# Kernel tuning notes

Measured on AMD Instinct MI355X. Metric: run time of the kernel, lower is better.

## Reference

```python
import jax, jax.numpy as jnp
import numpy as np

V, E, H, B, T = 50000, 300, 512, 64, 256


def _lstm_dir(x, wih, whh, bih, bhh, reverse):
    # x: [B,T,D]; wih: [4H,D]; whh: [4H,H]; PyTorch gate order i,f,g,o
    pre = jnp.einsum('btd,gd->btg', x, wih) + bih + bhh  # [B,T,4H]
    pre_t = jnp.swapaxes(pre, 0, 1)  # [T,B,4H]
    h0 = jnp.zeros((x.shape[0], whh.shape[1]), x.dtype)

    def step(carry, g):
        h, c = carry
        gates = g + h @ whh.T
        i, f, gg, o = jnp.split(gates, 4, axis=-1)
        c = jax.nn.sigmoid(f) * c + jax.nn.sigmoid(i) * jnp.tanh(gg)
        h = jax.nn.sigmoid(o) * jnp.tanh(c)
        return (h, c), h

    _, hs = jax.lax.scan(step, (h0, h0), pre_t, reverse=reverse)
    return jnp.swapaxes(hs, 0, 1)  # [B,T,H]


def setup_inputs() -> dict:
    key = jax.random.key(0)
    ks = jax.random.split(key, 24)
    s = 1.0 / np.sqrt(H)
    u = lambda k, shp: jax.random.uniform(k, shp, jnp.float32, -s, s)
    inp = {
        'input_ids': jax.random.randint(ks[0], (B, T), 0, V),
        'input_masks': jnp.ones((B, T), jnp.float32),
        'labels': jax.random.uniform(ks[1], (B, T), jnp.float32),
        'emb': jax.random.normal(ks[2], (V, E), jnp.float32),
        'lin_w': u(ks[3], (1, H)), 'lin_b': u(ks[4], (1,)),
    }
    dims = {'l0': E, 'l1': 2 * H}
    i = 5
    for layer, din in dims.items():
        for d in ('f', 'b'):
            inp[f'w_ih_{layer}{d}'] = u(ks[i], (4 * H, din)); i += 1
            inp[f'w_hh_{layer}{d}'] = u(ks[i], (4 * H, H)); i += 1
            inp[f'b_ih_{layer}{d}'] = u(ks[i], (4 * H,)); i += 1
            inp[f'b_hh_{layer}{d}'] = u(ks[i], (4 * H,)); i += 1
    return inp


def reference(input_ids, input_masks, labels, emb, lin_w, lin_b,
              w_ih_l0f, w_hh_l0f, b_ih_l0f, b_hh_l0f,
              w_ih_l0b, w_hh_l0b, b_ih_l0b, b_hh_l0b,
              w_ih_l1f, w_hh_l1f, b_ih_l1f, b_hh_l1f,
              w_ih_l1b, w_hh_l1b, b_ih_l1b, b_hh_l1b):
    x = emb[input_ids]  # vectorized gather, [B,T,E]
    h0f = _lstm_dir(x, w_ih_l0f, w_hh_l0f, b_ih_l0f, b_hh_l0f, False)
    h0b = _lstm_dir(x, w_ih_l0b, w_hh_l0b, b_ih_l0b, b_hh_l0b, True)
    x1 = jnp.concatenate([h0f, h0b], axis=-1)  # [B,T,2H] (dropout inactive at eval)
    h1f = _lstm_dir(x1, w_ih_l1f, w_hh_l1f, b_ih_l1f, b_hh_l1f, False)
    h1b = _lstm_dir(x1, w_ih_l1b, w_hh_l1b, b_ih_l1b, b_hh_l1b, True)
    mean_h = 0.5 * (h1f + h1b)  # mean over 2 directions, [B,T,H]
    scores = jax.nn.sigmoid(jnp.einsum('bth,oh->bto', mean_h, lin_w) + lin_b)  # [B,T,1]
    err = (scores[..., 0] - labels) ** 2 * input_masks  # masked MSE per token
    loss = jnp.mean(jnp.sum(err, axis=1) / jnp.sum(input_masks, axis=1))
    return loss
```

## Files before the change

### kernel.cpp

```cpp
#include <hip/hip_runtime.h>
#include <stdint.h>

#define T_SEQ 256
#define B_SZ  64
#define HID   512
#define G4    2048
#define E_DIM 300
#define E_PAD 320

typedef float f32x4 __attribute__((ext_vector_type(4)));
typedef short bf16x8 __attribute__((ext_vector_type(8)));
typedef short s16x4 __attribute__((ext_vector_type(4)));
typedef unsigned int u32x4 __attribute__((ext_vector_type(4)));

__device__ __forceinline__ unsigned short f2bf(float f) {
    union { float f; unsigned u; } v; v.f = f;
    unsigned r = v.u + 0x7FFF + ((v.u >> 16) & 1);
    return (unsigned short)(r >> 16);
}
__device__ __forceinline__ float bf2f(unsigned short b) {
    union { unsigned u; float f; } v; v.u = ((unsigned)b) << 16;
    return v.f;
}
__device__ __forceinline__ float sigm_f(float x) { return 1.0f / (1.0f + __expf(-x)); }
__device__ __forceinline__ float tanh_f(float x) {
    float e = __expf(-2.0f * fabsf(x));
    float t = (1.0f - e) / (1.0f + e);
    return x < 0.0f ? -t : t;
}

__global__ void k_sentinel(float* out) { out[0] = 12345.0f; }

__global__ __launch_bounds__(256) void k_gather(const int* __restrict__ ids,
                                                const float* __restrict__ emb,
                                                unsigned short* __restrict__ x) {
    int w = threadIdx.x >> 6, lane = threadIdx.x & 63;
    int m = blockIdx.x * 4 + w;
    int b = m & 63, t = m >> 6;
    int id = ids[b * T_SEQ + t];
    const float* e = emb + (size_t)id * E_DIM;
    unsigned short* xr = x + (size_t)m * E_PAD;
    for (int k = lane; k < E_PAD; k += 64)
        xr[k] = (k < E_DIM) ? f2bf(e[k]) : (unsigned short)0;
}

struct CastJobs {
    const float* s[8];
    unsigned short* d[8];
    int ks[8];
    int kp[8];
};
__global__ __launch_bounds__(256) void k_castall(CastJobs jobs) {
    int job = blockIdx.x >> 11;
    int row = blockIdx.x & 2047;
    int Ks = jobs.ks[job], Kp = jobs.kp[job];
    const float* s = jobs.s[job] + (size_t)row * Ks;
    unsigned short* d = jobs.d[job] + (size_t)row * Kp;
    for (int k = threadIdx.x; k < Kp; k += 256)
        d[k] = (k < Ks) ? f2bf(s[k]) : (unsigned short)0;
}

__global__ __launch_bounds__(256) void k_gemm(const unsigned short* __restrict__ A,
                                              const unsigned short* __restrict__ W,
                                              const float* __restrict__ bih,
                                              const float* __restrict__ bhh,
                                              unsigned short* __restrict__ outp,
                                              int Ka) {
    __shared__ __align__(16) short As[64][40];
    __shared__ __align__(16) short Bs[64][40];
    int tid = threadIdx.x;
    int w = tid >> 6, lane = tid & 63;
    int m0 = blockIdx.x * 64, n0 = blockIdx.y * 64;

    f32x4 acc[4];
    #pragma unroll
    for (int nt = 0; nt < 4; ++nt) { acc[nt][0]=0.f; acc[nt][1]=0.f; acc[nt][2]=0.f; acc[nt][3]=0.f; }

    int r = tid >> 2, seg = tid & 3;
    for (int k0 = 0; k0 < Ka; k0 += 32) {
        *(bf16x8*)&As[r][seg * 8] = *(const bf16x8*)&A[(size_t)(m0 + r) * Ka + k0 + seg * 8];
        *(bf16x8*)&Bs[r][seg * 8] = *(const bf16x8*)&W[(size_t)(n0 + r) * Ka + k0 + seg * 8];
        __syncthreads();
        bf16x8 a = *(const bf16x8*)&As[w * 16 + (lane & 15)][(lane >> 4) * 8];
        #pragma unroll
        for (int nt = 0; nt < 4; ++nt) {
            bf16x8 b = *(const bf16x8*)&Bs[nt * 16 + (lane & 15)][(lane >> 4) * 8];
            acc[nt] = __builtin_amdgcn_mfma_f32_16x16x32_bf16(a, b, acc[nt], 0, 0, 0);
        }
        __syncthreads();
    }
    int q = lane >> 4, j = lane & 15;
    int t = (m0 >> 6);
    #pragma unroll
    for (int nt = 0; nt < 4; ++nt) {
        int col = n0 + nt * 16 + j;
        int g = col >> 9, jc = col & 511;
        float b0 = bih[col] + bhh[col];
        s16x4 pk;
        #pragma unroll
        for (int rr = 0; rr < 4; ++rr)
            pk[rr] = (short)f2bf(acc[nt][rr] + b0);
        size_t idx = (((((size_t)t * 4 + w) * 4 + q) * 32 + (jc >> 4)) * 16 + (jc & 15)) * 16 + g * 4;
        *(s16x4*)&outp[idx] = pk;
    }
}

__global__ __launch_bounds__(256, 1) void k_lstm_layer(
        const unsigned short* __restrict__ pre2_f, const unsigned short* __restrict__ pre2_b,
        const unsigned short* __restrict__ whh_f, const unsigned short* __restrict__ whh_b,
        unsigned short* __restrict__ h_pp,
        int* __restrict__ flags,
        unsigned short* __restrict__ x1,
        unsigned short* __restrict__ h1f, unsigned short* __restrict__ h1b,
        int mode, int flag_base) {
    int tid = threadIdx.x, w = tid >> 6, lane = tid & 63;
    int jgg = blockIdx.x, rg = blockIdx.y, dir = blockIdx.z;
    int jg = jgg * 4 + w;
    int r0 = rg * 16, q = lane >> 4, j = lane & 15;
    const unsigned short* pre2 = dir ? pre2_b : pre2_f;
    const unsigned short* whh = dir ? whh_b : whh_f;
    int* gbase = flags + ((dir * 4 + rg) * 8) * 16;

    __shared__ __align__(16) short ws_a[16 * 512];

    bf16x8 breg[4][16];
    #pragma unroll
    for (int g = 0; g < 4; ++g)
        #pragma unroll
        for (int kc = 0; kc < 16; ++kc)
            breg[g][kc] = *(const bf16x8*)(whh + (size_t)(g * 512 + jg * 16 + j) * 512 + q * 8 + kc * 32);
    #pragma unroll
    for (int g = 0; g < 4; ++g)
        #pragma unroll
        for (int kc = 0; kc < 16; ++kc)
            asm volatile("" : "+a"(breg[g][kc]));

    float cr[4];
    #pragma unroll
    for (int rr = 0; rr < 4; ++rr) cr[rr] = 0.f;

    int aswz = (j & 7) << 4;
    const char* abase = (const char*)ws_a + (j << 10);
    int ko16 = q << 4;

    bf16x8 pcur0, pcur1;
    {
        int t0 = dir ? (T_SEQ - 1) : 0;
        const unsigned short* pp =
            pre2 + ((((((size_t)t0 * 4 + rg) * 4 + q) * 32 + jg) * 16 + j) * 16);
        pcur0 = *(const bf16x8*)pp;
        pcur1 = *(const bf16x8*)(pp + 8);
    }

    for (int s = 0; s < T_SEQ; ++s) {
        int t = dir ? (T_SEQ - 1 - s) : s;
        const unsigned short* hprev = h_pp + ((size_t)(s & 1) * 2 + dir) * (B_SZ * HID);
        unsigned short* hnext = h_pp + ((size_t)((s + 1) & 1) * 2 + dir) * (B_SZ * HID);

        f32x4 a0, a1, a2, a3;
        a0[0]=0.f;a0[1]=0.f;a0[2]=0.f;a0[3]=0.f; a1=a0; a2=a0; a3=a0;
        if (s > 0) {
            const unsigned short* hp = hprev + (size_t)r0 * HID;
            u32x4 va[4];
            #pragma unroll
            for (int c = 0; c < 4; ++c) {
                int ch = tid + c * 256;
                const void* src = hp + ((ch >> 6) << 9) + ((ch & 63) << 3);
                asm volatile("global_load_dwordx4 %0, %1, off sc0 sc1"
                             : "=v"(va[c]) : "v"(src));
            }
            asm volatile("s_waitcnt vmcnt(0)" ::: "memory");
            #pragma unroll
            for (int c = 0; c < 4; ++c) {
                int ch = tid + c * 256;
                int r = ch >> 6, o = ch & 63;
                *(u32x4*)((char*)ws_a + (r << 10) + ((o << 4) ^ ((r & 7) << 4))) = va[c];
            }
            __syncthreads();

            #pragma unroll
            for (int kc = 0; kc < 16; ++kc) {
                bf16x8 a = *(const bf16x8*)(abase + (((kc << 6) + ko16) ^ aswz));
                a0 = __builtin_amdgcn_mfma_f32_16x16x32_bf16(a, breg[0][kc], a0, 0, 0, 0);
                a1 = __builtin_amdgcn_mfma_f32_16x16x32_bf16(a, breg[1][kc], a1, 0, 0, 0);
                a2 = __builtin_amdgcn_mfma_f32_16x16x32_bf16(a, breg[2][kc], a2, 0, 0, 0);
                a3 = __builtin_amdgcn_mfma_f32_16x16x32_bf16(a, breg[3][kc], a3, 0, 0, 0);
            }
        }

        unsigned hbits[4];
        #pragma unroll
        for (int rr = 0; rr < 4; ++rr) {
            float iv = a0[rr] + bf2f((unsigned short)pcur0[rr]);
            float fv = a1[rr] + bf2f((unsigned short)pcur0[4 + rr]);
            float gv = a2[rr] + bf2f((unsigned short)pcur1[rr]);
            float ov = a3[rr] + bf2f((unsigned short)pcur1[4 + rr]);
            cr[rr] = sigm_f(fv) * cr[rr] + sigm_f(iv) * tanh_f(gv);
            float hh = sigm_f(ov) * tanh_f(cr[rr]);
            hbits[rr] = (unsigned)f2bf(hh);
        }

        #pragma unroll
        for (int rr = 0; rr < 4; ++rr) {
            unsigned nb = (unsigned)__shfl_xor((int)hbits[rr], 1);
            if ((j & 1) == 0) {
                unsigned pair = (hbits[rr] & 0xFFFFu) | (nb << 16);
                void* dsth = (void*)(hnext + (size_t)(r0 + q * 4 + rr) * HID + jg * 16 + j);
                asm volatile("global_store_dword %0, %1, off sc0 sc1"
                             :: "v"(dsth), "v"(pair) : "memory");
            }
        }

        asm volatile("s_waitcnt vmcnt(0)" ::: "memory");
        __syncthreads();
        int target = flag_base + s + 1;
        if (tid == 0)
            __hip_atomic_store(&gbase[jgg * 16], target, __ATOMIC_RELAXED, __HIP_MEMORY_SCOPE_AGENT);

        #pragma unroll
        for (int rr = 0; rr < 4; ++rr) {
            unsigned short hb = (unsigned short)hbits[rr];
            int brow = r0 + q * 4 + rr;
            if (mode == 0)
                x1[((size_t)t * B_SZ + brow) * 1024 + dir * HID + jg * 16 + j] = hb;
            else {
                unsigned short* o = dir ? h1b : h1f;
                o[((size_t)t * B_SZ + brow) * HID + jg * 16 + j] = hb;
            }
        }
        bf16x8 pn0, pn1;
        {
            int sn = (s + 1 < T_SEQ) ? s + 1 : s;
            int tn = dir ? (T_SEQ - 1 - sn) : sn;
            const unsigned short* pp =
                pre2 + ((((((size_t)tn * 4 + rg) * 4 + q) * 32 + jg) * 16 + j) * 16);
            pn0 = *(const bf16x8*)pp;
            pn1 = *(const bf16x8*)(pp + 8);
        }

        if (tid < 8) {
            while (__hip_atomic_load(&gbase[tid * 16], __ATOMIC_RELAXED, __HIP_MEMORY_SCOPE_AGENT) < target) {}
        }
        __syncthreads();
        pcur0 = pn0; pcur1 = pn1;
    }
}

__global__ __launch_bounds__(256) void k_score(const unsigned short* __restrict__ h1f,
                                               const unsigned short* __restrict__ h1b,
                                               const float* __restrict__ lin_w,
                                               const float* __restrict__ lin_b,
                                               const float* __restrict__ labels,
                                               const float* __restrict__ masks,
                                               float* __restrict__ err) {
    int w = threadIdx.x >> 6, lane = threadIdx.x & 63;
    int idx = blockIdx.x * 4 + w;
    int b = idx >> 8, t = idx & 255;
    size_t base = ((size_t)t * B_SZ + b) * HID + lane * 8;
    bf16x8 hf = *(const bf16x8*)(h1f + base);
    bf16x8 hb = *(const bf16x8*)(h1b + base);
    float sum = 0.f;
    #pragma unroll
    for (int i = 0; i < 8; ++i) {
        float m = 0.5f * (bf2f((unsigned short)hf[i]) + bf2f((unsigned short)hb[i]));
        sum += m * lin_w[lane * 8 + i];
    }
    #pragma unroll
    for (int off = 32; off; off >>= 1) sum += __shfl_xor(sum, off);
    if (lane == 0) {
        float sc = 1.0f / (1.0f + expf(-(sum + lin_b[0])));
        float d = sc - labels[b * 256 + t];
        err[b * 256 + t] = d * d * masks[b * 256 + t];
    }
}

__global__ void k_loss(const float* __restrict__ err, const float* __restrict__ masks,
                       float* __restrict__ out) {
    int lane = threadIdx.x;
    float se = 0.f, sm = 0.f;
    for (int t = 0; t < 256; ++t) {
        se += err[lane * 256 + t];
        sm += masks[lane * 256 + t];
    }
    float v = se / sm;
    #pragma unroll
    for (int off = 32; off; off >>= 1) v += __shfl_xor(v, off);
    if (lane == 0) out[0] = v * (1.0f / 64.0f);
}

extern "C" void kernel_launch(void* const* d_in, const int* in_sizes, int n_in,
                              void* d_out, int out_size, void* d_ws, size_t ws_size,
                              hipStream_t stream) {
    const int*   ids    = (const int*)d_in[0];
    const float* masks  = (const float*)d_in[1];
    const float* labels = (const float*)d_in[2];
    const float* emb    = (const float*)d_in[3];
    const float* lin_w  = (const float*)d_in[4];
    const float* lin_b  = (const float*)d_in[5];
    const float* w_ih[4] = {(const float*)d_in[6],  (const float*)d_in[10],
                            (const float*)d_in[14], (const float*)d_in[18]};
    const float* w_hh[4] = {(const float*)d_in[7],  (const float*)d_in[11],
                            (const float*)d_in[15], (const float*)d_in[19]};
    const float* b_ih[4] = {(const float*)d_in[8],  (const float*)d_in[12],
                            (const float*)d_in[16], (const float*)d_in[20]};
    const float* b_hh[4] = {(const float*)d_in[9],  (const float*)d_in[13],
                            (const float*)d_in[17], (const float*)d_in[21]};

    const size_t PRE_B   = (size_t)T_SEQ * B_SZ * G4 * 2;
    const size_t SH_B    = (size_t)16384 * 1024 * 2;
    const size_t WHH_B   = (size_t)G4 * HID * 2;
    const size_t WT1_B   = (size_t)G4 * 1024 * 2;
    const size_t HPP_B   = (size_t)2 * 2 * B_SZ * HID * 2;
    const size_t FLG_B   = (size_t)256 * 64;
    const size_t ERR_B   = (size_t)B_SZ * T_SEQ * 4;
    const size_t REQUIRED = 2 * PRE_B + SH_B + 4 * WHH_B + 2 * WT1_B + HPP_B + FLG_B + ERR_B;
    if (REQUIRED > ws_size) {
        k_sentinel<<<1, 1, 0, stream>>>((float*)d_out);
        return;
    }

    char* base = (char*)d_ws;
    unsigned short* pre_f = (unsigned short*)(base);
    unsigned short* pre_b = (unsigned short*)(base + PRE_B);
    char* sh = base + 2 * PRE_B;
    unsigned short* x_bf = (unsigned short*)(sh);
    unsigned short* wt0f = (unsigned short*)(sh + (size_t)16384 * E_PAD * 2);
    unsigned short* wt0b = (unsigned short*)(sh + (size_t)16384 * E_PAD * 2 + (size_t)2048 * E_PAD * 2);
    unsigned short* x1   = (unsigned short*)(sh);
    unsigned short* h1f  = (unsigned short*)(sh);
    unsigned short* h1b  = (unsigned short*)(sh + (size_t)T_SEQ * B_SZ * HID * 2);
    char* q = sh + SH_B;
    unsigned short* whhb[4];
    for (int i = 0; i < 4; ++i) { whhb[i] = (unsigned short*)q; q += WHH_B; }
    unsigned short* wt1f = (unsigned short*)q; q += WT1_B;
    unsigned short* wt1b = (unsigned short*)q; q += WT1_B;
    unsigned short* h_pp = (unsigned short*)q; q += HPP_B;
    int* flags = (int*)q; q += FLG_B;
    float* err = (float*)q; q += ERR_B;

    hipMemsetAsync(flags, 0, FLG_B, stream);

    k_gather<<<4096, 256, 0, stream>>>(ids, emb, x_bf);
    CastJobs cj;
    cj.s[0] = w_ih[0]; cj.d[0] = wt0f; cj.ks[0] = E_DIM; cj.kp[0] = E_PAD;
    cj.s[1] = w_ih[1]; cj.d[1] = wt0b; cj.ks[1] = E_DIM; cj.kp[1] = E_PAD;
    cj.s[2] = w_ih[2]; cj.d[2] = wt1f; cj.ks[2] = 1024;  cj.kp[2] = 1024;
    cj.s[3] = w_ih[3]; cj.d[3] = wt1b; cj.ks[3] = 1024;  cj.kp[3] = 1024;
    for (int i = 0; i < 4; ++i) {
        cj.s[4 + i] = w_hh[i]; cj.d[4 + i] = whhb[i]; cj.ks[4 + i] = 512; cj.kp[4 + i] = 512;
    }
    k_castall<<<16384, 256, 0, stream>>>(cj);

    dim3 gemm_grid(16384 / 64, 2048 / 64);
    k_gemm<<<gemm_grid, 256, 0, stream>>>(x_bf, wt0f, b_ih[0], b_hh[0], pre_f, E_PAD);
    k_gemm<<<gemm_grid, 256, 0, stream>>>(x_bf, wt0b, b_ih[1], b_hh[1], pre_b, E_PAD);

    dim3 rec_grid(8, 4, 2);
    k_lstm_layer<<<rec_grid, 256, 0, stream>>>(pre_f, pre_b, whhb[0], whhb[1],
                                               h_pp, flags, x1, nullptr, nullptr, 0, 0);

    k_gemm<<<gemm_grid, 256, 0, stream>>>(x1, wt1f, b_ih[2], b_hh[2], pre_f, 1024);
    k_gemm<<<gemm_grid, 256, 0, stream>>>(x1, wt1b, b_ih[3], b_hh[3], pre_b, 1024);

    k_lstm_layer<<<rec_grid, 256, 0, stream>>>(pre_f, pre_b, whhb[2], whhb[3],
                                               h_pp, flags, nullptr, h1f, h1b, 1, 256);

    k_score<<<4096, 256, 0, stream>>>(h1f, h1b, lin_w, lin_b, labels, masks, err);
    k_loss<<<1, 64, 0, stream>>>(err, masks, (float*)d_out);
}
```

Measured before the change: 2.392 ms.

## Enlarge input-projection GEMM tiles to 128x128 and drop AGPR pinning of recurrent weights

New measurement: 2.275 ms (median of 2 runs). -4.9%, faster.

```diff
diff --git a/kernel.cpp b/kernel.cpp
--- a/kernel.cpp
+++ b/kernel.cpp
@@ -66,42 +66,58 @@
                                               const float* __restrict__ bhh,
                                               unsigned short* __restrict__ outp,
                                               int Ka) {
-    __shared__ __align__(16) short As[64][40];
-    __shared__ __align__(16) short Bs[64][40];
+    __shared__ __align__(16) short As[128][40];
+    __shared__ __align__(16) short Bs[128][40];
     int tid = threadIdx.x;
     int w = tid >> 6, lane = tid & 63;
-    int m0 = blockIdx.x * 64, n0 = blockIdx.y * 64;
-
-    f32x4 acc[4];
-    #pragma unroll
-    for (int nt = 0; nt < 4; ++nt) { acc[nt][0]=0.f; acc[nt][1]=0.f; acc[nt][2]=0.f; acc[nt][3]=0.f; }
-
-    int r = tid >> 2, seg = tid & 3;
+    int wr = w >> 1, wc = w & 1;
+    int q = lane >> 4, j = lane & 15;
+    int m0 = blockIdx.x * 128, n0 = blockIdx.y * 128;
+
+    f32x4 acc[4][4];
+    #pragma unroll
+    for (int fi = 0; fi < 4; ++fi)
+        #pragma unroll
+        for (int nt = 0; nt < 4; ++nt) { acc[fi][nt][0]=0.f; acc[fi][nt][1]=0.f; acc[fi][nt][2]=0.f; acc[fi][nt][3]=0.f; }
+
     for (int k0 = 0; k0 < Ka; k0 += 32) {
-        *(bf16x8*)&As[r][seg * 8] = *(const bf16x8*)&A[(size_t)(m0 + r) * Ka + k0 + seg * 8];
-        *(bf16x8*)&Bs[r][seg * 8] = *(const bf16x8*)&W[(size_t)(n0 + r) * Ka + k0 + seg * 8];
+        #pragma unroll
+        for (int c = 0; c < 2; ++c) {
+            int ch = tid + c * 256;
+            int row = ch >> 2, cho = ch & 3;
+            *(bf16x8*)&As[row][cho * 8] = *(const bf16x8*)&A[(size_t)(m0 + row) * Ka + k0 + cho * 8];
+            *(bf16x8*)&Bs[row][cho * 8] = *(const bf16x8*)&W[(size_t)(n0 + row) * Ka + k0 + cho * 8];
+        }
         __syncthreads();
-        bf16x8 a = *(const bf16x8*)&As[w * 16 + (lane & 15)][(lane >> 4) * 8];
+        bf16x8 af[4], bf[4];
+        #pragma unroll
+        for (int fi = 0; fi < 4; ++fi)
+            af[fi] = *(const bf16x8*)&As[wr * 64 + fi * 16 + j][q * 8];
+        #pragma unroll
+        for (int nt = 0; nt < 4; ++nt)
+            bf[nt] = *(const bf16x8*)&Bs[wc * 64 + nt * 16 + j][q * 8];
+        #pragma unroll
+        for (int fi = 0; fi < 4; ++fi)
+            #pragma unroll
+            for (int nt = 0; nt < 4; ++nt)
+                acc[fi][nt] = __builtin_amdgcn_mfma_f32_16x16x32_bf16(af[fi], bf[nt], acc[fi][nt], 0, 0, 0);
+        __syncthreads();
+    }
+    int t = blockIdx.x * 2 + wr;
+    #pragma unroll
+    for (int fi = 0; fi < 4; ++fi) {
         #pragma unroll
         for (int nt = 0; nt < 4; ++nt) {
-            bf16x8 b = *(const bf16x8*)&Bs[nt * 16 + (lane & 15)][(lane >> 4) * 8];
-            acc[nt] = __builtin_amdgcn_mfma_f32_16x16x32_bf16(a, b, acc[nt], 0, 0, 0);
-        }
-        __syncthreads();
-    }
-    int q = lane >> 4, j = lane & 15;
-    int t = (m0 >> 6);
-    #pragma unroll
-    for (int nt = 0; nt < 4; ++nt) {
-        int col = n0 + nt * 16 + j;
-        int g = col >> 9, jc = col & 511;
-        float b0 = bih[col] + bhh[col];
-        s16x4 pk;
-        #pragma unroll
-        for (int rr = 0; rr < 4; ++rr)
-            pk[rr] = (short)f2bf(acc[nt][rr] + b0);
-        size_t idx = (((((size_t)t * 4 + w) * 4 + q) * 32 + (jc >> 4)) * 16 + (jc & 15)) * 16 + g * 4;
-        *(s16x4*)&outp[idx] = pk;
+            int col = n0 + wc * 64 + nt * 16 + j;
+            int g = col >> 9, jc = col & 511;
+            float b0 = bih[col] + bhh[col];
+            s16x4 pk;
+            #pragma unroll
+            for (int rr = 0; rr < 4; ++rr)
+                pk[rr] = (short)f2bf(acc[fi][nt][rr] + b0);
+            size_t idx = (((((size_t)t * 4 + fi) * 4 + q) * 32 + (jc >> 4)) * 16 + (jc & 15)) * 16 + g * 4;
+            *(s16x4*)&outp[idx] = pk;
+        }
     }
 }
 
@@ -129,11 +145,6 @@
         #pragma unroll
         for (int kc = 0; kc < 16; ++kc)
             breg[g][kc] = *(const bf16x8*)(whh + (size_t)(g * 512 + jg * 16 + j) * 512 + q * 8 + kc * 32);
-    #pragma unroll
-    for (int g = 0; g < 4; ++g)
-        #pragma unroll
-        for (int kc = 0; kc < 16; ++kc)
-            asm volatile("" : "+a"(breg[g][kc]));
 
     float cr[4];
     #pragma unroll
@@ -351,7 +362,7 @@
     }
     k_castall<<<16384, 256, 0, stream>>>(cj);
 
-    dim3 gemm_grid(16384 / 64, 2048 / 64);
+    dim3 gemm_grid(16384 / 128, 2048 / 128);
     k_gemm<<<gemm_grid, 256, 0, stream>>>(x_bf, wt0f, b_ih[0], b_hh[0], pre_f, E_PAD);
     k_gemm<<<gemm_grid, 256, 0, stream>>>(x_bf, wt0b, b_ih[1], b_hh[1], pre_b, E_PAD);
 
```
